# Performance work log

Hardware: AMD Instinct MI355X
Metric: run time of the kernel (lower is better)

## Reference

```python
import jax, jax.numpy as jnp
import numpy as np

B, C, H, W = 8, 80, 128, 128
K = 32          # objects per image (gt_obj_mask value)
HW = H * W
RES = 1e-4      # 'residual' constant in the torch code
PULL_W, PUSH_W, OFF_W = 0.1, 0.1, 1.0


def setup_inputs() -> dict:
    key = jax.random.key(0)
    ks = jax.random.split(key, 12)
    tl_heats = jax.random.normal(ks[0], (B, C, H, W), jnp.float32)
    br_heats = jax.random.normal(ks[1], (B, C, H, W), jnp.float32)
    tl_embeds = jax.random.normal(ks[2], (B, 1, H, W), jnp.float32)
    br_embeds = jax.random.normal(ks[3], (B, 1, H, W), jnp.float32)
    tl_offsets = jax.random.normal(ks[4], (B, 2, H, W), jnp.float32)
    br_offsets = jax.random.normal(ks[5], (B, 2, H, W), jnp.float32)
    gt_tl_offsets = jax.random.uniform(ks[6], (B, 2, H, W), jnp.float32)
    gt_br_offsets = jax.random.uniform(ks[7], (B, 2, H, W), jnp.float32)
    # object-id position maps: each id 1..K placed at exactly one distinct pixel
    k_ar = jnp.arange(K)
    b_ar = jnp.arange(B)[:, None]
    tl_idx = (k_ar[None, :] * 131 + b_ar * 7) % HW   # [B,K], distinct per batch
    br_idx = (k_ar[None, :] * 173 + b_ar * 11 + 5) % HW
    ids = jnp.broadcast_to(k_ar[None, :] + 1, (B, K)).astype(jnp.int32)
    gt_tl_pos = jnp.zeros((B, HW), jnp.int32).at[b_ar, tl_idx].set(ids).reshape(B, H, W)
    gt_br_pos = jnp.zeros((B, HW), jnp.int32).at[b_ar, br_idx].set(ids).reshape(B, H, W)
    # gt heatmaps in [0, 0.99], with exact 1.0 at corner pixels of class 0
    gt_tl_heats = (jax.random.uniform(ks[8], (B, C, HW), jnp.float32) * 0.99)
    gt_tl_heats = gt_tl_heats.at[b_ar, 0, tl_idx].set(1.0).reshape(B, C, H, W)
    gt_br_heats = (jax.random.uniform(ks[9], (B, C, HW), jnp.float32) * 0.99)
    gt_br_heats = gt_br_heats.at[b_ar, 0, br_idx].set(1.0).reshape(B, C, H, W)
    gt_obj_mask = jnp.full((B,), K, jnp.int32)
    return {
        "tl_heats": tl_heats, "tl_embeds": tl_embeds, "tl_offsets": tl_offsets,
        "br_heats": br_heats, "br_embeds": br_embeds, "br_offsets": br_offsets,
        "gt_tl_heats": gt_tl_heats, "gt_br_heats": gt_br_heats,
        "gt_tl_offsets": gt_tl_offsets, "gt_br_offsets": gt_br_offsets,
        "gt_tl_pos": gt_tl_pos, "gt_br_pos": gt_br_pos, "gt_obj_mask": gt_obj_mask,
    }


def _focal(logits, gt):
    # refined focal loss, alpha=2, beta=4, summed over batch
    p = jnp.clip(jax.nn.sigmoid(logits), RES, 1.0 - RES)
    pos = gt == 1.0
    pos_loss = jnp.where(pos, (1.0 - p) ** 2 * jnp.log(p), 0.0).sum(axis=(1, 2, 3))
    neg_loss = jnp.where(pos, 0.0, (1.0 - gt) ** 4 * p ** 2 * jnp.log(1.0 - p)).sum(axis=(1, 2, 3))
    num_pos = pos.sum(axis=(1, 2, 3)).astype(logits.dtype)  # >0 by construction
    return (-(pos_loss + neg_loss) / num_pos).sum()


def _offset(pred, gt, pos, objf):
    # smooth-L1 (beta=1, sum) over pixels where pos!=0, per batch / (obj+RES)
    m = (pos != 0).astype(pred.dtype)[:, None]          # [B,1,H,W]
    d = jnp.abs(pred - gt)
    l = jnp.where(d < 1.0, 0.5 * d * d, d - 0.5)
    per_b = (l * m).sum(axis=(1, 2, 3))
    return (per_b / (objf + RES)).sum()


def _gather_obj(emb, pos):
    # per-object embedding value (one pixel per id); index 0 forced to 0
    v = emb.reshape(B, HW)
    p = pos.reshape(B, HW)
    per = jax.vmap(lambda vv, pp: jax.ops.segment_sum(vv, pp, num_segments=K + 1))(v, p)
    return per.at[:, 0].set(0.0)   # [B, K+1] == torch's cat([0], gathered)


def reference(tl_heats, tl_embeds, tl_offsets, br_heats, br_embeds, br_offsets,
              gt_tl_heats, gt_br_heats, gt_tl_offsets, gt_br_offsets,
              gt_tl_pos, gt_br_pos, gt_obj_mask):
    objf = gt_obj_mask.astype(jnp.float32)              # [B]
    focal = _focal(tl_heats, gt_tl_heats) + _focal(br_heats, gt_br_heats)
    off = _offset(tl_offsets, gt_tl_offsets, gt_tl_pos, objf) \
        + _offset(br_offsets, gt_br_offsets, gt_br_pos, objf)
    tl_list = _gather_obj(tl_embeds, gt_tl_pos)         # [B, K+1]
    br_list = _gather_obj(br_embeds, gt_br_pos)
    mean = 0.5 * (tl_list + br_list)
    pull = ((((tl_list - mean) ** 2 + (br_list - mean) ** 2).sum(axis=1)) / (objf + RES)).sum()
    m = mean[:, 1:]                                     # [B, K]
    D = jax.nn.relu(1.0 - jnp.abs(m[:, :, None] - m[:, None, :]))
    dist = D.sum(axis=(1, 2)) - objf                    # -1 per diagonal term
    push = (dist / (objf * (objf - 1.0) + RES)).sum()
    total = focal + OFF_W * off + PULL_W * pull + PUSH_W * push
    return (total / B).reshape(1)
```

## Files before the change

### kernel.cpp

```cpp
#include <hip/hip_runtime.h>

#define BB 8
#define CC 80
#define HH 128
#define WWW 128
#define KK 32

constexpr int HWc  = HH * WWW;
constexpr int CHWc = CC * HWc;
constexpr float RESf   = 1e-4f;
constexpr float PULL_W = 0.1f;
constexpr float PUSH_W = 0.1f;
constexpr float OFF_W  = 1.0f;
constexpr float XCLAMP = 9.210240f;

typedef float f32x4 __attribute__((ext_vector_type(4)));

constexpr int WS_FLOATS = 6 * BB + 2 * BB * (KK + 1);

constexpr int NSML = 192;
constexpr int NFOC = 1024;
constexpr int NTOT = NSML + NFOC;

__device__ __forceinline__ void waveReduce2(float& a, float& b) {
#pragma unroll
    for (int off = 32; off; off >>= 1) {
        a += __shfl_down(a, off);
        b += __shfl_down(b, off);
    }
}

__device__ __forceinline__ float waveReduce1(float a) {
#pragma unroll
    for (int off = 32; off; off >>= 1) a += __shfl_down(a, off);
    return a;
}

__device__ __forceinline__ float aload(float* p) { return atomicAdd(p, 0.0f); }

__global__ __launch_bounds__(256) void loss_kernel(
    const float* __restrict__ tl, const float* __restrict__ gtl,
    const float* __restrict__ br, const float* __restrict__ gbr,
    const float* __restrict__ tlo, const float* __restrict__ gtlo,
    const float* __restrict__ bro, const float* __restrict__ gbro,
    const float* __restrict__ tle, const float* __restrict__ bre,
    const int* __restrict__ tpos, const int* __restrict__ bpos,
    const int* __restrict__ gt_obj_mask,
    float* ws, float* out) {
    __shared__ float sred[4], sred2[4];
    __shared__ bool is_last;

    const int bid = blockIdx.x;
    const int t = threadIdx.x;

    if (bid < NSML) {
        const int x = bid % 12;
        const int b = (bid / 12) % BB;
        const int z = bid / (12 * BB);
        const int* pos = (z ? bpos : tpos) + (size_t)b * HWc;
        const int4* pos4 = (const int4*)pos;

        if (x < 8) {
            const f32x4* pr4 = (const f32x4*)((z ? bro : tlo) + (size_t)b * 2 * HWc);
            const f32x4* gt4 = (const f32x4*)((z ? gbro : gtlo) + (size_t)b * 2 * HWc);
            const int n4 = 2 * HWc / 4;
            const int hw4n = HWc / 4;
            float sacc = 0.f;
            for (int i = x * 256 + t; i < n4; i += 8 * 256) {
                int hw4 = i & (hw4n - 1);
                f32x4 pv = __builtin_nontemporal_load(pr4 + i);
                f32x4 gv = __builtin_nontemporal_load(gt4 + i);
                int4 pp = pos4[hw4];
                int ms[4] = {pp.x, pp.y, pp.z, pp.w};
#pragma unroll
                for (int j = 0; j < 4; ++j) {
                    float d = fabsf(pv[j] - gv[j]);
                    float l = (d < 1.f) ? 0.5f * d * d : d - 0.5f;
                    sacc += (ms[j] != 0) ? l : 0.f;
                }
            }
            sacc = waveReduce1(sacc);
            if ((t & 63) == 0) sred[t >> 6] = sacc;
            __syncthreads();
            if (t == 0)
                atomicAdd(&ws[4 * BB + z * BB + b],
                          sred[0] + sred[1] + sred[2] + sred[3]);
        } else {
            const f32x4* e4 = (const f32x4*)((z ? bre : tle) + (size_t)b * HWc);
            float* list = ws + 6 * BB + z * BB * (KK + 1) + b * (KK + 1);
            const int n4 = HWc / 4;
            for (int i = (x - 8) * 256 + t; i < n4; i += 4 * 256) {
                f32x4 ev = __builtin_nontemporal_load(e4 + i);
                int4 pv = pos4[i];
                if (pv.x) atomicAdd(&list[pv.x], ev[0]);
                if (pv.y) atomicAdd(&list[pv.y], ev[1]);
                if (pv.z) atomicAdd(&list[pv.z], ev[2]);
                if (pv.w) atomicAdd(&list[pv.w], ev[3]);
            }
        }
    } else {
        const int r = bid - NSML;
        const int x = r & 63;
        const int b = (r >> 6) & 7;
        const int z = r >> 9;
        const f32x4* lg4 = (const f32x4*)((z ? br : tl) + (size_t)b * CHWc);
        const f32x4* gt4 = (const f32x4*)((z ? gbr : gtl) + (size_t)b * CHWc);
        float* lsum = ws + z * 2 * BB;
        float* npos = lsum + BB;

        constexpr int S = 64 * 256;
        constexpr int U = 4;
        constexpr int MACRO = CHWc / 4 / (U * S);
        const int tid = x * 256 + t;

        float ls = 0.f, np = 0.f;
#pragma unroll 1
        for (int m = 0; m < MACRO; ++m) {
            const int base = m * U * S + tid;
            f32x4 xv[U], gv[U];
#pragma unroll
            for (int u = 0; u < U; ++u) {
                xv[u] = __builtin_nontemporal_load(lg4 + base + u * S);
                gv[u] = __builtin_nontemporal_load(gt4 + base + u * S);
            }
#pragma unroll
            for (int u = 0; u < U; ++u) {
#pragma unroll
                for (int j = 0; j < 4; ++j) {
                    float xx = xv[u][j], g = gv[u][j];
                    float xc = fminf(fmaxf(xx, -XCLAMP), XCLAMP);
                    float e = __expf(xc);
                    float rr = __builtin_amdgcn_rcpf(1.f + e);
                    float p = e * rr;
                    float logq = __logf(rr);
                    float logp = xc + logq;
                    bool pos = (g == 1.0f);
                    float om = 1.f - g;
                    float om2 = om * om;
                    float v = pos ? rr * rr * logp
                                  : om2 * om2 * p * p * logq;
                    ls += v;
                    np += pos ? 1.f : 0.f;
                }
            }
        }
        waveReduce2(ls, np);
        if ((t & 63) == 0) { sred[t >> 6] = ls; sred2[t >> 6] = np; }
        __syncthreads();
        if (t == 0) {
            atomicAdd(&lsum[b], sred[0] + sred[1] + sred[2] + sred[3]);
            atomicAdd(&npos[b], sred2[0] + sred2[1] + sred2[2] + sred2[3]);
        }
    }

    asm volatile("s_waitcnt vmcnt(0)" ::: "memory");
    __syncthreads();
    if (t == 0) {
        unsigned* cnt = (unsigned*)(ws + WS_FLOATS);
        unsigned old = atomicAdd(cnt, 1u);
        is_last = (old == (unsigned)(NTOT - 1));
    }
    __syncthreads();
    if (!is_last) return;

    __shared__ float tls[BB * (KK + 1)], brs[BB * (KK + 1)], mns[BB * (KK + 1)];
    __shared__ float objf[BB];
    if (t < BB) objf[t] = (float)gt_obj_mask[t];
    float* wtl = ws + 6 * BB;
    float* wbr = wtl + BB * (KK + 1);
    for (int i = t; i < BB * (KK + 1); i += 256) {
        int k = i % (KK + 1);
        float a = (k == 0) ? 0.f : aload(&wtl[i]);
        float c = (k == 0) ? 0.f : aload(&wbr[i]);
        tls[i] = a; brs[i] = c; mns[i] = 0.5f * (a + c);
    }
    __syncthreads();

    float acc = 0.f;
    for (int i = t; i < BB * (KK + 1); i += 256) {
        int b = i / (KK + 1);
        float m = mns[i];
        float d1 = tls[i] - m, d2 = brs[i] - m;
        acc += PULL_W * (d1 * d1 + d2 * d2) / (objf[b] + RESf);
    }
    for (int i = t; i < BB * KK * KK; i += 256) {
        int b = i / (KK * KK);
        int r = i % (KK * KK);
        int ii = r / KK, jj = r % KK;
        float mi = mns[b * (KK + 1) + 1 + ii];
        float mj = mns[b * (KK + 1) + 1 + jj];
        float d = 1.f - fabsf(mi - mj);
        float D = d > 0.f ? d : 0.f;
        acc += PUSH_W * D / (objf[b] * (objf[b] - 1.f) + RESf);
    }
    for (int b = t; b < BB; b += 256) {
        float of = objf[b];
        acc += -aload(&ws[b]) / aload(&ws[BB + b]);
        acc += -aload(&ws[2 * BB + b]) / aload(&ws[3 * BB + b]);
        acc += OFF_W * aload(&ws[4 * BB + b]) / (of + RESf);
        acc += OFF_W * aload(&ws[5 * BB + b]) / (of + RESf);
        acc += -PUSH_W * of / (of * (of - 1.f) + RESf);
    }

    acc = waveReduce1(acc);
    __syncthreads();
    if ((t & 63) == 0) sred[t >> 6] = acc;
    __syncthreads();
    if (t == 0) out[0] = (sred[0] + sred[1] + sred[2] + sred[3]) / (float)BB;
}

extern "C" void kernel_launch(void* const* d_in, const int* in_sizes, int n_in,
                              void* d_out, int out_size, void* d_ws, size_t ws_size,
                              hipStream_t stream) {
    const float* tl_heats      = (const float*)d_in[0];
    const float* tl_embeds     = (const float*)d_in[1];
    const float* tl_offsets    = (const float*)d_in[2];
    const float* br_heats      = (const float*)d_in[3];
    const float* br_embeds     = (const float*)d_in[4];
    const float* br_offsets    = (const float*)d_in[5];
    const float* gt_tl_heats   = (const float*)d_in[6];
    const float* gt_br_heats   = (const float*)d_in[7];
    const float* gt_tl_offsets = (const float*)d_in[8];
    const float* gt_br_offsets = (const float*)d_in[9];
    const int*   gt_tl_pos     = (const int*)d_in[10];
    const int*   gt_br_pos     = (const int*)d_in[11];
    const int*   gt_obj_mask   = (const int*)d_in[12];
    float* out = (float*)d_out;
    float* ws  = (float*)d_ws;

    hipMemsetAsync(ws, 0, (WS_FLOATS + 1) * sizeof(float), stream);

    loss_kernel<<<dim3(NTOT), 256, 0, stream>>>(
        tl_heats, gt_tl_heats, br_heats, gt_br_heats,
        tl_offsets, gt_tl_offsets, br_offsets, gt_br_offsets,
        tl_embeds, br_embeds, gt_tl_pos, gt_br_pos,
        gt_obj_mask, ws, out);
}
```

Before: 53.49 us.

## Fold small offset/embed work into focal blocks, removing separate block group

Instead of dedicating 192 extra blocks to offset and embedding reductions, the grid is reduced to 1024 blocks. Each block first handles one small chunk: blocks 0-511 process one f32x4 of offset loss and blocks 512-767 one f32x4 of embedding scatter. Every block then runs its focal-loss slice. This removes the tail of separate small blocks and balances work across the focal grid, at the cost of an extra sync and atomic in the first 512 blocks and uneven per-block work.

New measurement: 55.78 us. 1.04x slower.

```diff
diff --git a/kernel.cpp b/kernel.cpp
--- a/kernel.cpp
+++ b/kernel.cpp
@@ -18,9 +18,7 @@
 
 constexpr int WS_FLOATS = 6 * BB + 2 * BB * (KK + 1);
 
-constexpr int NSML = 192;
-constexpr int NFOC = 1024;
-constexpr int NTOT = NSML + NFOC;
+constexpr int NTOT = 1024;
 
 __device__ __forceinline__ void waveReduce2(float& a, float& b) {
 #pragma unroll
@@ -47,62 +45,58 @@
     const int* __restrict__ tpos, const int* __restrict__ bpos,
     const int* __restrict__ gt_obj_mask,
     float* ws, float* out) {
-    __shared__ float sred[4], sred2[4];
+    __shared__ float sred[4], sred2[4], ssml[4];
     __shared__ bool is_last;
 
     const int bid = blockIdx.x;
     const int t = threadIdx.x;
 
-    if (bid < NSML) {
-        const int x = bid % 12;
-        const int b = (bid / 12) % BB;
-        const int z = bid / (12 * BB);
-        const int* pos = (z ? bpos : tpos) + (size_t)b * HWc;
-        const int4* pos4 = (const int4*)pos;
-
-        if (x < 8) {
-            const f32x4* pr4 = (const f32x4*)((z ? bro : tlo) + (size_t)b * 2 * HWc);
-            const f32x4* gt4 = (const f32x4*)((z ? gbro : gtlo) + (size_t)b * 2 * HWc);
-            const int n4 = 2 * HWc / 4;
-            const int hw4n = HWc / 4;
-            float sacc = 0.f;
-            for (int i = x * 256 + t; i < n4; i += 8 * 256) {
-                int hw4 = i & (hw4n - 1);
-                f32x4 pv = __builtin_nontemporal_load(pr4 + i);
-                f32x4 gv = __builtin_nontemporal_load(gt4 + i);
-                int4 pp = pos4[hw4];
-                int ms[4] = {pp.x, pp.y, pp.z, pp.w};
-#pragma unroll
-                for (int j = 0; j < 4; ++j) {
-                    float d = fabsf(pv[j] - gv[j]);
-                    float l = (d < 1.f) ? 0.5f * d * d : d - 0.5f;
-                    sacc += (ms[j] != 0) ? l : 0.f;
-                }
-            }
-            sacc = waveReduce1(sacc);
-            if ((t & 63) == 0) sred[t >> 6] = sacc;
-            __syncthreads();
-            if (t == 0)
-                atomicAdd(&ws[4 * BB + z * BB + b],
-                          sred[0] + sred[1] + sred[2] + sred[3]);
-        } else {
-            const f32x4* e4 = (const f32x4*)((z ? bre : tle) + (size_t)b * HWc);
-            float* list = ws + 6 * BB + z * BB * (KK + 1) + b * (KK + 1);
-            const int n4 = HWc / 4;
-            for (int i = (x - 8) * 256 + t; i < n4; i += 4 * 256) {
-                f32x4 ev = __builtin_nontemporal_load(e4 + i);
-                int4 pv = pos4[i];
-                if (pv.x) atomicAdd(&list[pv.x], ev[0]);
-                if (pv.y) atomicAdd(&list[pv.y], ev[1]);
-                if (pv.z) atomicAdd(&list[pv.z], ev[2]);
-                if (pv.w) atomicAdd(&list[pv.w], ev[3]);
-            }
+    if (bid < 512) {
+        const int i = bid * 256 + t;
+        const int z = i >> 16;
+        const int b = (i >> 13) & 7;
+        const int k = i & 8191;
+        const int hw4 = k & 4095;
+        const f32x4* pr4 = (const f32x4*)((z ? bro : tlo) + (size_t)b * 2 * HWc);
+        const f32x4* gt4 = (const f32x4*)((z ? gbro : gtlo) + (size_t)b * 2 * HWc);
+        const int4* pos4 = (const int4*)((z ? bpos : tpos) + (size_t)b * HWc);
+        f32x4 pv = __builtin_nontemporal_load(pr4 + k);
+        f32x4 gv = __builtin_nontemporal_load(gt4 + k);
+        int4 pp = pos4[hw4];
+        int ms[4] = {pp.x, pp.y, pp.z, pp.w};
+        float sacc = 0.f;
+#pragma unroll
+        for (int j = 0; j < 4; ++j) {
+            float d = fabsf(pv[j] - gv[j]);
+            float l = (d < 1.f) ? 0.5f * d * d : d - 0.5f;
+            sacc += (ms[j] != 0) ? l : 0.f;
         }
-    } else {
-        const int r = bid - NSML;
-        const int x = r & 63;
-        const int b = (r >> 6) & 7;
-        const int z = r >> 9;
+        sacc = waveReduce1(sacc);
+        if ((t & 63) == 0) ssml[t >> 6] = sacc;
+        __syncthreads();
+        if (t == 0)
+            atomicAdd(&ws[4 * BB + z * BB + b],
+                      ssml[0] + ssml[1] + ssml[2] + ssml[3]);
+    } else if (bid < 768) {
+        const int j = (bid - 512) * 256 + t;
+        const int z = j >> 15;
+        const int b = (j >> 12) & 7;
+        const int k = j & 4095;
+        const f32x4* e4 = (const f32x4*)((z ? bre : tle) + (size_t)b * HWc);
+        const int4* pos4 = (const int4*)((z ? bpos : tpos) + (size_t)b * HWc);
+        f32x4 ev = __builtin_nontemporal_load(e4 + k);
+        int4 pv = pos4[k];
+        float* list = ws + 6 * BB + z * BB * (KK + 1) + b * (KK + 1);
+        if (pv.x) atomicAdd(&list[pv.x], ev[0]);
+        if (pv.y) atomicAdd(&list[pv.y], ev[1]);
+        if (pv.z) atomicAdd(&list[pv.z], ev[2]);
+        if (pv.w) atomicAdd(&list[pv.w], ev[3]);
+    }
+
+    {
+        const int x = bid & 63;
+        const int b = (bid >> 6) & 7;
+        const int z = bid >> 9;
         const f32x4* lg4 = (const f32x4*)((z ? br : tl) + (size_t)b * CHWc);
         const f32x4* gt4 = (const f32x4*)((z ? gbr : gtl) + (size_t)b * CHWc);
         float* lsum = ws + z * 2 * BB;
```
